# Kernel optimization log

Hardware: AMD Instinct MI355X
Metric: run time of the kernel (lower is better)

The kernel has to match this reference:

```python
import jax, jax.numpy as jnp
import numpy as np

N_NODES, N_EDGES, MAX_NB = 40000, 80000, 4
INPUT_SIZE, NODE_FDIM, HIDDEN = 384, 256, 256
DEPTH = 6


def setup_inputs() -> dict:
    key = jax.random.key(0)
    ks = jax.random.split(key, 16)
    s = 0.05  # weight init scale
    return {
        "fnode": jax.random.normal(ks[0], (N_NODES, NODE_FDIM), dtype=jnp.float32),
        "fmess": jax.random.normal(ks[1], (N_EDGES, INPUT_SIZE), dtype=jnp.float32),
        "agraph": jax.random.randint(ks[2], (N_NODES, MAX_NB), 0, N_EDGES),
        "bgraph": jax.random.randint(ks[3], (N_EDGES, MAX_NB), 0, N_EDGES),
        "mask": jnp.ones((N_NODES, 1), dtype=jnp.float32),
        "Wz": jax.random.normal(ks[4], (INPUT_SIZE + HIDDEN, HIDDEN), dtype=jnp.float32) * s,
        "bz": jnp.zeros((HIDDEN,), dtype=jnp.float32),
        "Wr": jax.random.normal(ks[5], (INPUT_SIZE, HIDDEN), dtype=jnp.float32) * s,
        "Ur": jax.random.normal(ks[6], (HIDDEN, HIDDEN), dtype=jnp.float32) * s,
        "bur": jnp.zeros((HIDDEN,), dtype=jnp.float32),
        "Wh": jax.random.normal(ks[7], (INPUT_SIZE + HIDDEN, HIDDEN), dtype=jnp.float32) * s,
        "bh": jnp.zeros((HIDDEN,), dtype=jnp.float32),
        "Wo": jax.random.normal(ks[8], (NODE_FDIM + HIDDEN, HIDDEN), dtype=jnp.float32) * s,
        "bo": jnp.zeros((HIDDEN,), dtype=jnp.float32),
        "depth": DEPTH,
    }


def reference(fnode, fmess, agraph, bgraph, mask, Wz, bz, Wr, Ur, bur, Wh, bh, Wo, bo, depth):
    E, H = fmess.shape[0], Wz.shape[1]
    # message 0 is padding -> kept at zero each step (mask[0,0]=0 in torch GRU)
    msg_mask = jnp.ones((E, 1), dtype=fmess.dtype).at[0, 0].set(0.0)
    rx = fmess @ Wr  # precomputable: [E, H], reset gate input term

    def step(h, _):
        h_nei = h[bgraph]                      # [E, nb, H] gather
        sum_h = h_nei.sum(axis=1)              # [E, H]
        z = jax.nn.sigmoid(jnp.concatenate([fmess, sum_h], axis=1) @ Wz + bz)
        r = jax.nn.sigmoid(rx[:, None, :] + h_nei @ Ur + bur)  # [E, nb, H]
        sum_gh = (r * h_nei).sum(axis=1)
        pre_h = jnp.tanh(jnp.concatenate([fmess, sum_gh], axis=1) @ Wh + bh)
        h_new = ((1.0 - z) * sum_h + z * pre_h) * msg_mask
        return h_new, None

    h0 = jnp.zeros((E, H), dtype=fmess.dtype)
    h, _ = jax.lax.scan(step, h0, None, length=depth)

    nei_message = h[agraph].sum(axis=1)        # [N, H] gather-sum over incoming edges
    node_hiddens = jax.nn.relu(jnp.concatenate([fnode, nei_message], axis=1) @ Wo + bo)
    return node_hiddens * mask, h
```

## Files before the change

kernel.cpp:

```cpp
#include <hip/hip_runtime.h>
#include <stdint.h>

#define N_NODES 40000
#define N_EDGES 80000
#define HID 256
#define DEPTH_FIXED 6
#define NPAD 40064
#define MT 32

typedef __bf16 bf16;
typedef __bf16 bf16x4 __attribute__((ext_vector_type(4)));
typedef __bf16 bf16x8 __attribute__((ext_vector_type(8)));
typedef float f32x4 __attribute__((ext_vector_type(4)));

#define TPAD 136
#define APAD 264

__device__ __forceinline__ float sigmoidf_(float x) { return 1.f / (1.f + __expf(-x)); }
__device__ __forceinline__ float tanhf_(float x) { float e = __expf(2.f * x); return 1.f - 2.f / (e + 1.f); }

__device__ __forceinline__ void gld_lds16(const void* g, void* l) {
    __builtin_amdgcn_global_load_lds(
        (const __attribute__((address_space(1))) uint32_t*)g,
        (__attribute__((address_space(3))) uint32_t*)l, 16, 0, 0);
}

__device__ __forceinline__ void stage_tile(const bf16* __restrict__ src, int ld, int r0, int k0,
                                           bf16* lds, int tid) {
#pragma unroll
    for (int jj = 0; jj < 2; ++jj) {
        int s = jj * 256 + tid;
        int c = s ^ ((s >> 3) & 3);
        gld_lds16(src + (size_t)(r0 + (c >> 2)) * ld + k0 + (c & 3) * 8, lds + s * 8);
    }
}

__device__ __forceinline__ void mfma_tile(const bf16* lds_a, const bf16* lds_b,
                                          int wm, int wn, int lane, f32x4 (&acc)[4][4]) {
    const int li = lane & 15, quad = lane >> 4;
    const int sw = quad ^ ((li >> 1) & 3);
    bf16x8 a[4], b[4];
#pragma unroll
    for (int i = 0; i < 4; ++i)
        a[i] = *(const bf16x8*)(lds_a + ((wm * 64 + i * 16 + li) * 4 + sw) * 8);
#pragma unroll
    for (int j = 0; j < 4; ++j)
        b[j] = *(const bf16x8*)(lds_b + ((wn * 64 + j * 16 + li) * 4 + sw) * 8);
#pragma unroll
    for (int i = 0; i < 4; ++i)
#pragma unroll
        for (int j = 0; j < 4; ++j)
            acc[i][j] = __builtin_amdgcn_mfma_f32_16x16x32_bf16(a[i], b[j], acc[i][j], 0, 0, 0);
}

__global__ __launch_bounds__(256, 3) void step_fused_k(
    const int* __restrict__ bgraph, const bf16* __restrict__ Hcur,
    const bf16* __restrict__ HU, const bf16* __restrict__ P,
    const bf16* __restrict__ B1T, const bf16* __restrict__ B2T,
    bf16* __restrict__ Hnew, float* __restrict__ HF) {
    __shared__ __align__(16) bf16 sA1[MT * APAD];
    __shared__ __align__(16) bf16 sA2[MT * APAD];
    __shared__ __align__(16) bf16 sBst[256 * 32];
    const int tid = threadIdx.x, lane = tid & 63, wave = tid >> 6;
    const int m0 = blockIdx.x * MT;

    {
        const int r = tid >> 3, qc = tid & 7;
        const int e = m0 + r;
        const int4 nb = *(const int4*)(bgraph + (size_t)e * 4);
        const int bi[4] = {nb.x, nb.y, nb.z, nb.w};
        const bf16* prx = P + (size_t)e * 768 + qc * 32;
        bf16x8 rx[4];
#pragma unroll
        for (int c = 0; c < 4; ++c) rx[c] = *(const bf16x8*)(prx + c * 8);
        float sh[4][8] = {}, gh[4][8] = {};
#pragma unroll
        for (int j = 0; j < 4; ++j) {
            const bf16* hp = Hcur + (size_t)bi[j] * HID + qc * 32;
            const bf16* up = HU + (size_t)bi[j] * HID + qc * 32;
            bf16x8 hv[4], uv[4];
#pragma unroll
            for (int c = 0; c < 4; ++c) { hv[c] = *(const bf16x8*)(hp + c * 8); uv[c] = *(const bf16x8*)(up + c * 8); }
#pragma unroll
            for (int c = 0; c < 4; ++c)
#pragma unroll
                for (int u = 0; u < 8; ++u) {
                    float hf = (float)hv[c][u];
                    float rr = sigmoidf_((float)rx[c][u] + (float)uv[c][u]);
                    sh[c][u] += hf;
                    gh[c][u] += rr * hf;
                }
        }
#pragma unroll
        for (int c = 0; c < 4; ++c) {
            bf16x8 os, og;
#pragma unroll
            for (int u = 0; u < 8; ++u) { os[u] = (bf16)sh[c][u]; og[u] = (bf16)gh[c][u]; }
            *(bf16x8*)(sA1 + r * APAD + qc * 32 + c * 8) = os;
            *(bf16x8*)(sA2 + r * APAD + qc * 32 + c * 8) = og;
        }
    }
    __syncthreads();

    const int li = lane & 15, quad = lane >> 4;
    const int sw = quad ^ ((li >> 1) & 3);
    f32x4 accZ[2][4] = {}, accH[2][4] = {};
#pragma unroll
    for (int pass = 0; pass < 2; ++pass) {
        const bf16* BT = pass ? B2T : B1T;
        const bf16* sA = pass ? sA2 : sA1;
        for (int t = 0; t < 8; ++t) {
#pragma unroll
            for (int jj = 0; jj < 4; ++jj) {
                int s = jj * 256 + tid;
                int c = s ^ ((s >> 3) & 3);
                gld_lds16(BT + (size_t)(c >> 2) * 256 + t * 32 + (c & 3) * 8, sBst + s * 8);
            }
            __syncthreads();
            bf16x8 a[2], b[4];
#pragma unroll
            for (int i = 0; i < 2; ++i)
                a[i] = *(const bf16x8*)(sA + (i * 16 + li) * APAD + t * 32 + quad * 8);
#pragma unroll
            for (int j = 0; j < 4; ++j)
                b[j] = *(const bf16x8*)(sBst + ((wave * 64 + j * 16 + li) * 4 + sw) * 8);
#pragma unroll
            for (int i = 0; i < 2; ++i)
#pragma unroll
                for (int j = 0; j < 4; ++j) {
                    if (pass == 0) accZ[i][j] = __builtin_amdgcn_mfma_f32_16x16x32_bf16(a[i], b[j], accZ[i][j], 0, 0, 0);
                    else           accH[i][j] = __builtin_amdgcn_mfma_f32_16x16x32_bf16(a[i], b[j], accH[i][j], 0, 0, 0);
                }
            __syncthreads();
        }
    }

    bf16* tZ = sA2;
    bf16* tH = sBst;
#pragma unroll
    for (int i = 0; i < 2; ++i)
#pragma unroll
        for (int j = 0; j < 4; ++j) {
            const int col = wave * 64 + j * 16 + li;
#pragma unroll
            for (int r = 0; r < 4; ++r) {
                const int row = i * 16 + quad * 4 + r;
                tZ[row * APAD + col] = (bf16)accZ[i][j][r];
                tH[row * 256 + col] = (bf16)accH[i][j][r];
            }
        }
    __syncthreads();
#pragma unroll
    for (int s = 0; s < 4; ++s) {
        int v = s * 256 + tid;
        int lr = v >> 5, c8 = (v & 31) * 8;
        int e = m0 + lr;
        bf16x8 zl = *(const bf16x8*)(tZ + lr * APAD + c8);
        bf16x8 hl = *(const bf16x8*)(tH + lr * 256 + c8);
        bf16x8 shv = *(const bf16x8*)(sA1 + lr * APAD + c8);
        bf16x8 zx = *(const bf16x8*)(P + (size_t)e * 768 + 256 + c8);
        bf16x8 hx = *(const bf16x8*)(P + (size_t)e * 768 + 512 + c8);
        bf16x8 o;
        float of[8];
#pragma unroll
        for (int u = 0; u < 8; ++u) {
            float z = sigmoidf_((float)zl[u] + (float)zx[u]);
            float p = tanhf_((float)hl[u] + (float)hx[u]);
            float hn = (1.f - z) * (float)shv[u] + z * p;
            if (e == 0) hn = 0.f;
            o[u] = (bf16)hn;
            of[u] = hn;
        }
        *(bf16x8*)(Hnew + (size_t)e * HID + c8) = o;
        if (HF) {
            *(float4*)(HF + (size_t)e * HID + c8) = make_float4(of[0], of[1], of[2], of[3]);
            *(float4*)(HF + (size_t)e * HID + c8 + 4) = make_float4(of[4], of[5], of[6], of[7]);
        }
    }
}

__global__ __launch_bounds__(256) void gemm_single_k(
    const bf16* __restrict__ A, const bf16* __restrict__ BT,
    const float* __restrict__ bias, bf16* __restrict__ C, int K, int ldc) {
    __shared__ __align__(16) char smem[34816];
    bf16* sA = (bf16*)smem;
    bf16* sB = sA + 4096;
    const int tid = threadIdx.x, lane = tid & 63, wave = tid >> 6;
    const int wm = wave >> 1, wn = wave & 1;
    const int m0 = blockIdx.x * 128, n0 = blockIdx.y * 128;
    f32x4 acc[4][4] = {};
    for (int k0 = 0; k0 < K; k0 += 32) {
        stage_tile(A, K, m0, k0, sA, tid);
        stage_tile(BT, K, n0, k0, sB, tid);
        __syncthreads();
        mfma_tile(sA, sB, wm, wn, lane, acc);
        __syncthreads();
    }
    bf16* tC = (bf16*)smem;
#pragma unroll
    for (int i = 0; i < 4; ++i)
#pragma unroll
        for (int j = 0; j < 4; ++j) {
            const int col = wn * 64 + j * 16 + (lane & 15);
#pragma unroll
            for (int r = 0; r < 4; ++r) {
                const int lr = wm * 64 + i * 16 + (lane >> 4) * 4 + r;
                tC[lr * TPAD + col] = (bf16)acc[i][j][r];
            }
        }
    __syncthreads();
#pragma unroll
    for (int s = 0; s < 8; ++s) {
        int v = s * 256 + tid;
        int lr = v >> 4, c8 = (v & 15) * 8;
        bf16x8 cv = *(const bf16x8*)(tC + lr * TPAD + c8);
        bf16x8 o;
        if (bias) {
            float4 b0 = *(const float4*)(bias + n0 + c8);
            float4 b1 = *(const float4*)(bias + n0 + c8 + 4);
            o[0] = (bf16)((float)cv[0] + b0.x); o[1] = (bf16)((float)cv[1] + b0.y);
            o[2] = (bf16)((float)cv[2] + b0.z); o[3] = (bf16)((float)cv[3] + b0.w);
            o[4] = (bf16)((float)cv[4] + b1.x); o[5] = (bf16)((float)cv[5] + b1.y);
            o[6] = (bf16)((float)cv[6] + b1.z); o[7] = (bf16)((float)cv[7] + b1.w);
        } else {
            o = cv;
        }
        *(bf16x8*)(C + (size_t)(m0 + lr) * ldc + n0 + c8) = o;
    }
}

__global__ __launch_bounds__(256) void gemm_out_k(
    const bf16* __restrict__ A1, const bf16* __restrict__ A2,
    const bf16* __restrict__ B1T, const bf16* __restrict__ B2T,
    const float* __restrict__ bo, const float* __restrict__ mask, float* __restrict__ out) {
    __shared__ __align__(16) char smem[34816];
    bf16* s0 = (bf16*)smem;
    bf16* s1 = s0 + 4096;
    bf16* s2 = s1 + 4096;
    bf16* s3 = s2 + 4096;
    const int tid = threadIdx.x, lane = tid & 63, wave = tid >> 6;
    const int wm = wave >> 1, wn = wave & 1;
    const int m0 = blockIdx.x * 128, n0 = blockIdx.y * 128;
    f32x4 acc1[4][4] = {}, acc2[4][4] = {};
    for (int k0 = 0; k0 < 256; k0 += 32) {
        stage_tile(A1, 256, m0, k0, s0, tid);
        stage_tile(B1T, 256, n0, k0, s1, tid);
        stage_tile(A2, 256, m0, k0, s2, tid);
        stage_tile(B2T, 256, n0, k0, s3, tid);
        __syncthreads();
        mfma_tile(s0, s1, wm, wn, lane, acc1);
        mfma_tile(s2, s3, wm, wn, lane, acc2);
        __syncthreads();
    }
    bf16* tC = (bf16*)smem;
#pragma unroll
    for (int i = 0; i < 4; ++i)
#pragma unroll
        for (int j = 0; j < 4; ++j) {
            const int col = wn * 64 + j * 16 + (lane & 15);
#pragma unroll
            for (int r = 0; r < 4; ++r) {
                const int lr = wm * 64 + i * 16 + (lane >> 4) * 4 + r;
                tC[lr * TPAD + col] = (bf16)(acc1[i][j][r] + acc2[i][j][r]);
            }
        }
    __syncthreads();
#pragma unroll
    for (int s = 0; s < 8; ++s) {
        int v = s * 256 + tid;
        int lr = v >> 4, c8 = (v & 15) * 8;
        int grow = m0 + lr;
        if (grow >= N_NODES) continue;
        int gcol = n0 + c8;
        bf16x8 cv = *(const bf16x8*)(tC + lr * TPAD + c8);
        float4 b0 = *(const float4*)(bo + gcol);
        float4 b1 = *(const float4*)(bo + gcol + 4);
        float mk = mask[grow];
        float4 o0, o1;
        o0.x = fmaxf((float)cv[0] + b0.x, 0.f) * mk;
        o0.y = fmaxf((float)cv[1] + b0.y, 0.f) * mk;
        o0.z = fmaxf((float)cv[2] + b0.z, 0.f) * mk;
        o0.w = fmaxf((float)cv[3] + b0.w, 0.f) * mk;
        o1.x = fmaxf((float)cv[4] + b1.x, 0.f) * mk;
        o1.y = fmaxf((float)cv[5] + b1.y, 0.f) * mk;
        o1.z = fmaxf((float)cv[6] + b1.z, 0.f) * mk;
        o1.w = fmaxf((float)cv[7] + b1.w, 0.f) * mk;
        *(float4*)(out + (size_t)grow * 256 + gcol) = o0;
        *(float4*)(out + (size_t)grow * 256 + gcol + 4) = o1;
    }
}

__global__ __launch_bounds__(256) void gather_nei_k(
    const int* __restrict__ agraph, const bf16* __restrict__ H, bf16* __restrict__ nei) {
    int i = blockIdx.x * 256 + threadIdx.x;
    int v = i >> 5, c8 = (i & 31) * 8;
    bf16x8 o;
    if (v < N_NODES) {
        int4 nb = *(const int4*)(agraph + (size_t)v * 4);
        int bi[4] = {nb.x, nb.y, nb.z, nb.w};
        float s[8] = {};
#pragma unroll
        for (int j = 0; j < 4; ++j) {
            bf16x8 hv = *(const bf16x8*)(H + (size_t)bi[j] * HID + c8);
#pragma unroll
            for (int r = 0; r < 8; ++r) s[r] += (float)hv[r];
        }
#pragma unroll
        for (int r = 0; r < 8; ++r) o[r] = (bf16)s[r];
    } else {
#pragma unroll
        for (int r = 0; r < 8; ++r) o[r] = (bf16)0.f;
    }
    *(bf16x8*)(nei + (size_t)v * HID + c8) = o;
}

__global__ __launch_bounds__(256) void step1_k(const bf16* __restrict__ P, bf16* __restrict__ H) {
    int i = blockIdx.x * 256 + threadIdx.x;
    int e = i >> 5, c8 = (i & 31) * 8;
    bf16x8 zx = *(const bf16x8*)(P + (size_t)e * 768 + 256 + c8);
    bf16x8 hx = *(const bf16x8*)(P + (size_t)e * 768 + 512 + c8);
    bf16x8 o;
#pragma unroll
    for (int r = 0; r < 8; ++r) {
        float h = sigmoidf_((float)zx[r]) * tanhf_((float)hx[r]);
        if (e == 0) h = 0.f;
        o[r] = (bf16)h;
    }
    *(bf16x8*)(H + (size_t)e * HID + c8) = o;
}

__global__ void cvt_bf16_k(const float* __restrict__ src, bf16* __restrict__ dst, int n4) {
    int i = blockIdx.x * 256 + threadIdx.x;
    if (i >= n4) return;
    float4 v = ((const float4*)src)[i];
    bf16x4 o = {(bf16)v.x, (bf16)v.y, (bf16)v.z, (bf16)v.w};
    *((bf16x4*)dst + i) = o;
}

__global__ void cvt_fnode_k(const float* __restrict__ src, bf16* __restrict__ dst) {
    int i = blockIdx.x * 256 + threadIdx.x;
    int row = i >> 6;
    bf16x4 o = {(bf16)0.f, (bf16)0.f, (bf16)0.f, (bf16)0.f};
    if (row < N_NODES) {
        float4 v = ((const float4*)src)[i];
        o[0] = (bf16)v.x; o[1] = (bf16)v.y; o[2] = (bf16)v.z; o[3] = (bf16)v.w;
    }
    *((bf16x4*)dst + i) = o;
}

__global__ void prep_wpre_k(const float* __restrict__ Wr, const float* __restrict__ Wz,
                            const float* __restrict__ Wh, bf16* __restrict__ WT) {
    int idx = blockIdx.x * 256 + threadIdx.x;
    if (idx >= 768 * 384) return;
    int n = idx / 384, k = idx % 384;
    float v;
    if (n < 256) v = Wr[(size_t)k * 256 + n];
    else if (n < 512) v = Wz[(size_t)k * 256 + (n - 256)];
    else v = Wh[(size_t)k * 256 + (n - 512)];
    WT[idx] = (bf16)v;
}

__global__ void prep_bias_k(const float* __restrict__ bur, const float* __restrict__ bz,
                            const float* __restrict__ bh, float* __restrict__ bp) {
    int n = blockIdx.x * 256 + threadIdx.x;
    if (n >= 768) return;
    bp[n] = n < 256 ? bur[n] : (n < 512 ? bz[n - 256] : bh[n - 512]);
}

__global__ void prep_t256_k(const float* __restrict__ W, bf16* __restrict__ T, int roff) {
    int idx = blockIdx.x * 256 + threadIdx.x;
    int n = idx >> 8, k = idx & 255;
    T[idx] = (bf16)W[(size_t)(roff + k) * 256 + n];
}

extern "C" void kernel_launch(void* const* d_in, const int* in_sizes, int n_in,
                              void* d_out, int out_size, void* d_ws, size_t ws_size,
                              hipStream_t stream) {
    (void)in_sizes; (void)n_in; (void)out_size; (void)ws_size;
    const float* fnode = (const float*)d_in[0];
    const float* fmess = (const float*)d_in[1];
    const int* agraph = (const int*)d_in[2];
    const int* bgraph = (const int*)d_in[3];
    const float* mask = (const float*)d_in[4];
    const float* Wz = (const float*)d_in[5];
    const float* bz = (const float*)d_in[6];
    const float* Wr = (const float*)d_in[7];
    const float* Ur = (const float*)d_in[8];
    const float* bur = (const float*)d_in[9];
    const float* Wh = (const float*)d_in[10];
    const float* bh = (const float*)d_in[11];
    const float* Wo = (const float*)d_in[12];
    const float* bo = (const float*)d_in[13];
    float* out_node = (float*)d_out;
    float* out_h = out_node + (size_t)N_NODES * HID;

    char* ws = (char*)d_ws;
    size_t off = 0;
    auto alloc = [&](size_t b) -> char* { char* p = ws + off; off += (b + 255) & ~(size_t)255; return p; };
    bf16* P     = (bf16*)alloc((size_t)N_EDGES * 768 * 2);
    bf16* Hb0   = (bf16*)alloc((size_t)N_EDGES * HID * 2);
    bf16* Hb1   = (bf16*)alloc((size_t)N_EDGES * HID * 2);
    bf16* HU    = (bf16*)alloc((size_t)N_EDGES * HID * 2);
    bf16* fnodeB= (bf16*)alloc((size_t)NPAD * HID * 2);
    bf16* nei   = (bf16*)alloc((size_t)NPAD * HID * 2);
    bf16* WTpre = (bf16*)alloc((size_t)768 * 384 * 2);
    bf16* UrT   = (bf16*)alloc(65536 * 2);
    bf16* WzBT  = (bf16*)alloc(65536 * 2);
    bf16* WhBT  = (bf16*)alloc(65536 * 2);
    bf16* WoTT  = (bf16*)alloc(65536 * 2);
    bf16* WoBT  = (bf16*)alloc(65536 * 2);
    float* biasP= (float*)alloc(768 * 4);
    bf16* fmessB = Hb1;

    cvt_bf16_k<<<30000, 256, 0, stream>>>(fmess, fmessB, N_EDGES * 384 / 4);
    cvt_fnode_k<<<NPAD * 64 / 256, 256, 0, stream>>>(fnode, fnodeB);
    prep_wpre_k<<<(768 * 384 + 255) / 256, 256, 0, stream>>>(Wr, Wz, Wh, WTpre);
    prep_bias_k<<<3, 256, 0, stream>>>(bur, bz, bh, biasP);
    prep_t256_k<<<256, 256, 0, stream>>>(Ur, UrT, 0);
    prep_t256_k<<<256, 256, 0, stream>>>(Wz, WzBT, 384);
    prep_t256_k<<<256, 256, 0, stream>>>(Wh, WhBT, 384);
    prep_t256_k<<<256, 256, 0, stream>>>(Wo, WoTT, 0);
    prep_t256_k<<<256, 256, 0, stream>>>(Wo, WoBT, 256);

    gemm_single_k<<<dim3(625, 6), 256, 0, stream>>>(fmessB, WTpre, biasP, P, 384, 768);

    step1_k<<<N_EDGES * 32 / 256, 256, 0, stream>>>(P, Hb0);

    bf16* cur = Hb0;
    bf16* nxt = Hb1;
    for (int d = 2; d <= DEPTH_FIXED; ++d) {
        gemm_single_k<<<dim3(625, 2), 256, 0, stream>>>(cur, UrT, nullptr, HU, 256, 256);
        step_fused_k<<<N_EDGES / MT, 256, 0, stream>>>(bgraph, cur, HU, P, WzBT, WhBT, nxt,
                                                       d == DEPTH_FIXED ? out_h : nullptr);
        bf16* t = cur; cur = nxt; nxt = t;
    }

    gather_nei_k<<<NPAD * 32 / 256, 256, 0, stream>>>(agraph, cur, nei);
    gemm_out_k<<<dim3(313, 2), 256, 0, stream>>>(fnodeB, nei, WoTT, WoBT, bo, mask, out_node);
}
```

Measured before the change: 1.399 ms.

## Load pre-packed weight fragments directly from global in fused GRU step

```diff
diff --git a/kernel.cpp b/kernel.cpp
--- a/kernel.cpp
+++ b/kernel.cpp
@@ -53,14 +53,13 @@
             acc[i][j] = __builtin_amdgcn_mfma_f32_16x16x32_bf16(a[i], b[j], acc[i][j], 0, 0, 0);
 }
 
-__global__ __launch_bounds__(256, 3) void step_fused_k(
+__global__ __launch_bounds__(256, 4) void step_fused_k(
     const int* __restrict__ bgraph, const bf16* __restrict__ Hcur,
     const bf16* __restrict__ HU, const bf16* __restrict__ P,
-    const bf16* __restrict__ B1T, const bf16* __restrict__ B2T,
+    const bf16* __restrict__ B1P, const bf16* __restrict__ B2P,
     bf16* __restrict__ Hnew, float* __restrict__ HF) {
     __shared__ __align__(16) bf16 sA1[MT * APAD];
     __shared__ __align__(16) bf16 sA2[MT * APAD];
-    __shared__ __align__(16) bf16 sBst[256 * 32];
     const int tid = threadIdx.x, lane = tid & 63, wave = tid >> 6;
     const int m0 = blockIdx.x * MT;
 
@@ -103,27 +102,20 @@
     __syncthreads();
 
     const int li = lane & 15, quad = lane >> 4;
-    const int sw = quad ^ ((li >> 1) & 3);
     f32x4 accZ[2][4] = {}, accH[2][4] = {};
 #pragma unroll
     for (int pass = 0; pass < 2; ++pass) {
-        const bf16* BT = pass ? B2T : B1T;
         const bf16* sA = pass ? sA2 : sA1;
+        const bf16* bbase = (pass ? B2P : B1P) + (wave << 11) + (li << 5) + (quad << 3);
+#pragma unroll 2
         for (int t = 0; t < 8; ++t) {
-#pragma unroll
-            for (int jj = 0; jj < 4; ++jj) {
-                int s = jj * 256 + tid;
-                int c = s ^ ((s >> 3) & 3);
-                gld_lds16(BT + (size_t)(c >> 2) * 256 + t * 32 + (c & 3) * 8, sBst + s * 8);
-            }
-            __syncthreads();
             bf16x8 a[2], b[4];
 #pragma unroll
             for (int i = 0; i < 2; ++i)
                 a[i] = *(const bf16x8*)(sA + (i * 16 + li) * APAD + t * 32 + quad * 8);
 #pragma unroll
             for (int j = 0; j < 4; ++j)
-                b[j] = *(const bf16x8*)(sBst + ((wave * 64 + j * 16 + li) * 4 + sw) * 8);
+                b[j] = *(const bf16x8*)(bbase + (t << 13) + (j << 9));
 #pragma unroll
             for (int i = 0; i < 2; ++i)
 #pragma unroll
@@ -131,12 +123,18 @@
                     if (pass == 0) accZ[i][j] = __builtin_amdgcn_mfma_f32_16x16x32_bf16(a[i], b[j], accZ[i][j], 0, 0, 0);
                     else           accH[i][j] = __builtin_amdgcn_mfma_f32_16x16x32_bf16(a[i], b[j], accH[i][j], 0, 0, 0);
                 }
-            __syncthreads();
-        }
-    }
-
+        }
+    }
+
+    bf16x8 shv[4];
+#pragma unroll
+    for (int s = 0; s < 4; ++s) {
+        int v = s * 256 + tid;
+        shv[s] = *(const bf16x8*)(sA1 + (v >> 5) * APAD + (v & 31) * 8);
+    }
+    __syncthreads();
     bf16* tZ = sA2;
-    bf16* tH = sBst;
+    bf16* tH = sA1;
 #pragma unroll
     for (int i = 0; i < 2; ++i)
 #pragma unroll
@@ -146,7 +144,7 @@
             for (int r = 0; r < 4; ++r) {
                 const int row = i * 16 + quad * 4 + r;
                 tZ[row * APAD + col] = (bf16)accZ[i][j][r];
-                tH[row * 256 + col] = (bf16)accH[i][j][r];
+                tH[row * APAD + col] = (bf16)accH[i][j][r];
             }
         }
     __syncthreads();
@@ -156,8 +154,7 @@
         int lr = v >> 5, c8 = (v & 31) * 8;
         int e = m0 + lr;
         bf16x8 zl = *(const bf16x8*)(tZ + lr * APAD + c8);
-        bf16x8 hl = *(const bf16x8*)(tH + lr * 256 + c8);
-        bf16x8 shv = *(const bf16x8*)(sA1 + lr * APAD + c8);
+        bf16x8 hl = *(const bf16x8*)(tH + lr * APAD + c8);
         bf16x8 zx = *(const bf16x8*)(P + (size_t)e * 768 + 256 + c8);
         bf16x8 hx = *(const bf16x8*)(P + (size_t)e * 768 + 512 + c8);
         bf16x8 o;
@@ -166,7 +163,7 @@
         for (int u = 0; u < 8; ++u) {
             float z = sigmoidf_((float)zl[u] + (float)zx[u]);
             float p = tanhf_((float)hl[u] + (float)hx[u]);
-            float hn = (1.f - z) * (float)shv[u] + z * p;
+            float hn = (1.f - z) * (float)shv[s][u] + z * p;
             if (e == 0) hn = 0.f;
             o[u] = (bf16)hn;
             of[u] = hn;
@@ -373,6 +370,13 @@
     T[idx] = (bf16)W[(size_t)(roff + k) * 256 + n];
 }
 
+__global__ void prep_bpack_k(const float* __restrict__ W, bf16* __restrict__ Bp, int roff) {
+    int idx = blockIdx.x * 256 + threadIdx.x;
+    int n = idx >> 8, k = idx & 255;
+    int off = ((k >> 5) << 13) + ((n >> 4) << 9) + ((n & 15) << 5) + (k & 31);
+    Bp[off] = (bf16)W[(size_t)(roff + k) * 256 + n];
+}
+
 extern "C" void kernel_launch(void* const* d_in, const int* in_sizes, int n_in,
                               void* d_out, int out_size, void* d_ws, size_t ws_size,
                               hipStream_t stream) {
@@ -405,8 +409,8 @@
     bf16* nei   = (bf16*)alloc((size_t)NPAD * HID * 2);
     bf16* WTpre = (bf16*)alloc((size_t)768 * 384 * 2);
     bf16* UrT   = (bf16*)alloc(65536 * 2);
-    bf16* WzBT  = (bf16*)alloc(65536 * 2);
-    bf16* WhBT  = (bf16*)alloc(65536 * 2);
+    bf16* WzPK  = (bf16*)alloc(65536 * 2);
+    bf16* WhPK  = (bf16*)alloc(65536 * 2);
     bf16* WoTT  = (bf16*)alloc(65536 * 2);
     bf16* WoBT  = (bf16*)alloc(65536 * 2);
     float* biasP= (float*)alloc(768 * 4);
@@ -417,8 +421,8 @@
     prep_wpre_k<<<(768 * 384 + 255) / 256, 256, 0, stream>>>(Wr, Wz, Wh, WTpre);
     prep_bias_k<<<3, 256, 0, stream>>>(bur, bz, bh, biasP);
     prep_t256_k<<<256, 256, 0, stream>>>(Ur, UrT, 0);
-    prep_t256_k<<<256, 256, 0, stream>>>(Wz, WzBT, 384);
-    prep_t256_k<<<256, 256, 0, stream>>>(Wh, WhBT, 384);
+    prep_bpack_k<<<256, 256, 0, stream>>>(Wz, WzPK, 384);
+    prep_bpack_k<<<256, 256, 0, stream>>>(Wh, WhPK, 384);
     prep_t256_k<<<256, 256, 0, stream>>>(Wo, WoTT, 0);
     prep_t256_k<<<256, 256, 0, stream>>>(Wo, WoBT, 256);
 
@@ -430,7 +434,7 @@
     bf16* nxt = Hb1;
     for (int d = 2; d <= DEPTH_FIXED; ++d) {
         gemm_single_k<<<dim3(625, 2), 256, 0, stream>>>(cur, UrT, nullptr, HU, 256, 256);
-        step_fused_k<<<N_EDGES / MT, 256, 0, stream>>>(bgraph, cur, HU, P, WzBT, WhBT, nxt,
+        step_fused_k<<<N_EDGES / MT, 256, 0, stream>>>(bgraph, cur, HU, P, WzPK, WhPK, nxt,
                                                        d == DEPTH_FIXED ? out_h : nullptr);
         bf16* t = cur; cur = nxt; nxt = t;
     }
```

Result: slower. 1.579 ms (+12.8%).
